# Optimization experiments

Measured on AMD Instinct MI355X. Metric: run time of the kernel, lower is better.

Reference implementation:

```python
import jax, jax.numpy as jnp
import numpy as np

DIM = 1024
HEADS = 16
DIM_HEAD = 64


def setup_inputs() -> dict:
    key = jax.random.key(0)
    ks = jax.random.split(key, 6)
    b, n = 2, 2048
    x = jax.random.normal(ks[0], (b, n, DIM), dtype=jnp.float32)
    gamma = jnp.ones((DIM,), dtype=jnp.float32)
    w_qkv = jax.random.normal(ks[1], (DIM, 3 * HEADS * DIM_HEAD), dtype=jnp.float32) * (DIM ** -0.5)
    w_gates = jax.random.normal(ks[2], (DIM, HEADS), dtype=jnp.float32) * (DIM ** -0.5)
    b_gates = jnp.zeros((HEADS,), dtype=jnp.float32)
    w_out = jax.random.normal(ks[3], (HEADS * DIM_HEAD, DIM), dtype=jnp.float32) * ((HEADS * DIM_HEAD) ** -0.5)
    freqs = jax.random.uniform(ks[4], (DIM_HEAD // 2,), dtype=jnp.float32)
    return {"x": x, "gamma": gamma, "w_qkv": w_qkv, "w_gates": w_gates,
            "b_gates": b_gates, "w_out": w_out, "freqs": freqs}


def _rotate_half(t):
    # interleaved pairs: (x1, x2) -> (-x2, x1)
    tp = t.reshape(t.shape[:-1] + (t.shape[-1] // 2, 2))
    x1, x2 = tp[..., 0], tp[..., 1]
    return jnp.stack((-x2, x1), axis=-1).reshape(t.shape)


def reference(x, gamma, w_qkv, w_gates, b_gates, w_out, freqs):
    b, n, d = x.shape
    # RMSNorm variant: divide by L2 norm, scale by gamma * sqrt(dim)
    xn = x / jnp.linalg.norm(x, axis=-1, keepdims=True)
    xn = xn * gamma * (d ** 0.5)
    # QKV projection: (b, n, 3*H*D) -> q,k,v each (b, h, n, dh)
    qkv = xn @ w_qkv
    qkv = qkv.reshape(b, n, 3, HEADS, DIM_HEAD).transpose(2, 0, 3, 1, 4)
    q, k, v = qkv[0], qkv[1], qkv[2]
    # Inline RoPE (interleaved): freqs (n, dh)
    pos = jnp.arange(n, dtype=freqs.dtype)
    f = jnp.repeat(pos[:, None] * freqs[None, :], 2, axis=-1)  # (n, dh)
    cos_f, sin_f = jnp.cos(f), jnp.sin(f)
    q = q * cos_f + _rotate_half(q) * sin_f
    k = k * cos_f + _rotate_half(k) * sin_f
    # SDPA
    scale = DIM_HEAD ** -0.5
    scores = jnp.einsum('bhqd,bhkd->bhqk', q, k) * scale
    attn = jax.nn.softmax(scores, axis=-1)
    out = jnp.einsum('bhqk,bhkd->bhqd', attn, v)  # (b, h, n, dh)
    # per-head sigmoid gate from normalized input
    gates = xn @ w_gates + b_gates  # (b, n, h)
    out = out * jax.nn.sigmoid(gates.transpose(0, 2, 1))[..., None]
    # merge heads and output projection
    out = out.transpose(0, 2, 1, 3).reshape(b, n, HEADS * DIM_HEAD)
    return out @ w_out
```

## Files before the change

### kernel.cpp

```cpp
#include <hip/hip_runtime.h>

typedef __bf16 bf16_t;
typedef __bf16 bf16x8 __attribute__((ext_vector_type(8)));
typedef __bf16 bf16x4 __attribute__((ext_vector_type(4)));
typedef float f32x4 __attribute__((ext_vector_type(4)));

#define B_  2
#define N_  2048
#define D_  1024
#define H_  16
#define DH_ 64

#define QSCALE 0.18033688011112042f
#define NEGC  -11.541560327111707f

#if __has_builtin(__builtin_amdgcn_exp2f)
#define EXP2F(x) __builtin_amdgcn_exp2f(x)
#else
#define EXP2F(x) exp2f(x)
#endif

#define GLL16(g, l) __builtin_amdgcn_global_load_lds( \
    (const __attribute__((address_space(1))) void*)(g), \
    (__attribute__((address_space(3))) void*)(l), 16, 0, 0)

__device__ __forceinline__ int xcd_swizzle_id() {
  int id = blockIdx.y * gridDim.x + blockIdx.x;
  int cpx = (gridDim.x * gridDim.y) >> 3;
  return (id & 7) * cpx + (id >> 3);
}

__global__ __launch_bounds__(256) void k_prep(
    const float* __restrict__ x, const float* __restrict__ gamma,
    const float* __restrict__ wg, const float* __restrict__ bg,
    bf16_t* __restrict__ xn, float* __restrict__ gsig,
    const float* __restrict__ w_qkv, bf16_t* __restrict__ wqkvT,
    const float* __restrict__ w_out, bf16_t* __restrict__ woutT,
    const float* __restrict__ freqs, float* __restrict__ tc, float* __restrict__ ts) {
  __shared__ __align__(16) char smem_raw[17424];
  int id = blockIdx.x, tid = threadIdx.x;
  if (id < 4096) {
    float* red4 = (float*)smem_raw;
    float (*red)[17] = (float(*)[17])(smem_raw + 16);
    int row = id;
    const float4* xr = (const float4*)(x + (size_t)row * D_);
    float4 v = xr[tid];
    float ss = v.x*v.x + v.y*v.y + v.z*v.z + v.w*v.w;
    #pragma unroll
    for (int off = 32; off > 0; off >>= 1) ss += __shfl_down(ss, off);
    if ((tid & 63) == 0) red4[tid >> 6] = ss;
    __syncthreads();
    float scale = 32.0f * rsqrtf(red4[0] + red4[1] + red4[2] + red4[3]);
    float4 g = ((const float4*)gamma)[tid];
    bf16x4 o;
    o[0] = (bf16_t)(v.x * scale * g.x);
    o[1] = (bf16_t)(v.y * scale * g.y);
    o[2] = (bf16_t)(v.z * scale * g.z);
    o[3] = (bf16_t)(v.w * scale * g.w);
    *(bf16x4*)(xn + (size_t)row * D_ + tid * 4) = o;
    float xv[4] = {(float)o[0], (float)o[1], (float)o[2], (float)o[3]};
    float part[16];
    #pragma unroll
    for (int h = 0; h < 16; ++h) part[h] = 0.f;
    #pragma unroll
    for (int j = 0; j < 4; ++j) {
      const float4* wr = (const float4*)&wg[(size_t)(tid * 4 + j) * 16];
      #pragma unroll
      for (int q = 0; q < 4; ++q) {
        float4 w4 = wr[q];
        part[q * 4 + 0] += xv[j] * w4.x;
        part[q * 4 + 1] += xv[j] * w4.y;
        part[q * 4 + 2] += xv[j] * w4.z;
        part[q * 4 + 3] += xv[j] * w4.w;
      }
    }
    #pragma unroll
    for (int h = 0; h < 16; ++h) red[tid][h] = part[h];
    __syncthreads();
    int h = tid & 15, grp = tid >> 4;
    float s = 0.f;
    #pragma unroll
    for (int k = 0; k < 16; ++k) s += red[grp * 16 + k][h];
    __syncthreads();
    red[grp][h] = s;
    __syncthreads();
    if (tid < 16) {
      float acc = bg[tid];
      #pragma unroll
      for (int k = 0; k < 16; ++k) acc += red[k][tid];
      gsig[(size_t)row * 16 + tid] = 1.0f / (1.0f + __expf(-acc));
    }
  } else if (id < 8192) {
    const float* W; bf16_t* Wt; int R, C, bx, by;
    if (id < 7168) { int local = id - 4096; W = w_qkv; Wt = wqkvT; R = 1024; C = 3072;
                     bx = local % 96; by = local / 96; }
    else           { int local = id - 7168; W = w_out; Wt = woutT; R = 1024; C = 1024;
                     bx = local & 31; by = local >> 5; }
    float (*tile)[33] = (float(*)[33])smem_raw;
    int c0 = bx * 32, r0 = by * 32;
    int tx = tid & 31, ty = tid >> 5;
    #pragma unroll
    for (int i = 0; i < 4; ++i) {
      int r = ty + i * 8;
      tile[r][tx] = W[(size_t)(r0 + r) * C + c0 + tx];
    }
    __syncthreads();
    #pragma unroll
    for (int i = 0; i < 4; ++i) {
      int rr = ty + i * 8;
      Wt[(size_t)(c0 + rr) * R + r0 + tx] = (bf16_t)tile[tx][rr];
    }
  } else {
    int idx = (id - 8192) * 256 + tid;
    int n = idx >> 5, j = idx & 31;
    float f = (float)n * freqs[j];
    tc[idx] = cosf(f);
    ts[idx] = sinf(f);
  }
}

__global__ __launch_bounds__(256) void k_gemm_qkv(const bf16_t* __restrict__ A,
    const bf16_t* __restrict__ Bt, const float* __restrict__ tc,
    const float* __restrict__ ts, bf16_t* __restrict__ Qb,
    bf16_t* __restrict__ Kb, bf16_t* __restrict__ Vb) {
  constexpr int BK = 32, K = 1024;
  constexpr int TP = 136;
  __shared__ __align__(16) char smem[128 * TP * 2];
  bf16_t* As0 = (bf16_t*)smem;
  bf16_t* Bs0 = (bf16_t*)(smem + 16384);
  bf16_t* Tt  = (bf16_t*)smem;
  int tid = threadIdx.x, wave = tid >> 6, lane = tid & 63;
  int l16 = lane & 15, quad = lane >> 4;
  int id = blockIdx.y * 32 + blockIdx.x;
  int xcd = id & 7, local = id >> 3;
  int bxi = (xcd & 3) * 8 + (local & 7);
  int byi = (xcd >> 2) * 12 + (local >> 3);
  int bm = bxi * 128, bn = byi * 128;
  int wm = (wave >> 1) * 64, wn = (wave & 1) * 64;
  int srow = wave * 32 + (lane >> 2);
  int scol = (lane & 3) * 8;
  const bf16_t* gA0 = &A [(size_t)(bm + srow)      * K + scol];
  const bf16_t* gA1 = &A [(size_t)(bm + srow + 16) * K + scol];
  const bf16_t* gB0 = &Bt[(size_t)(bn + srow)      * K + scol];
  const bf16_t* gB1 = &Bt[(size_t)(bn + srow + 16) * K + scol];
  bf16_t* lA0 = &As0[(wave * 32)      * BK];
  bf16_t* lA1 = &As0[(wave * 32 + 16) * BK];
  bf16_t* lB0 = &Bs0[(wave * 32)      * BK];
  bf16_t* lB1 = &Bs0[(wave * 32 + 16) * BK];
  f32x4 acc[4][4] = {};
  GLL16(gA0, lA0); GLL16(gA1, lA1); GLL16(gB0, lB0); GLL16(gB1, lB1);
  __syncthreads();
  for (int k0 = 0; k0 < K; k0 += BK) {
    int cur = (k0 >> 5) & 1;
    int co  = cur * 4096;
    int nxt = 4096 - co;
    if (k0 + BK < K) {
      GLL16(gA0 + k0 + BK, lA0 + nxt);
      GLL16(gA1 + k0 + BK, lA1 + nxt);
      GLL16(gB0 + k0 + BK, lB0 + nxt);
      GLL16(gB1 + k0 + BK, lB1 + nxt);
    }
    const bf16_t* Asc = As0 + co;
    const bf16_t* Bsc = Bs0 + co;
    bf16x8 af[4], bfr[4];
    #pragma unroll
    for (int t = 0; t < 4; ++t) {
      af[t]  = *(const bf16x8*)&Asc[(wm + t * 16 + l16) * BK + quad * 8];
      bfr[t] = *(const bf16x8*)&Bsc[(wn + t * 16 + l16) * BK + quad * 8];
    }
    #pragma unroll
    for (int mt = 0; mt < 4; ++mt)
      #pragma unroll
      for (int nt = 0; nt < 4; ++nt)
        acc[mt][nt] = __builtin_amdgcn_mfma_f32_16x16x32_bf16(af[mt], bfr[nt], acc[mt][nt], 0, 0, 0);
    __syncthreads();
  }
  if (byi < 16) {
    float qs = (byi < 8) ? QSCALE : 1.0f;
    bf16_t* dst = (byi < 8) ? Qb : Kb;
    #pragma unroll
    for (int mt = 0; mt < 4; ++mt)
      #pragma unroll
      for (int r = 0; r < 4; ++r) {
        int row_l = wm + mt * 16 + quad * 4 + r;
        int n = (bm + row_l) & 2047;
        const float* cr = tc + n * 32;
        const float* sr = ts + n * 32;
        #pragma unroll
        for (int nt = 0; nt < 4; ++nt) {
          int col_l = wn + nt * 16 + l16;
          int d = (bn + col_l) & 63, j = d >> 1;
          float val = acc[mt][nt][r];
          float p = __shfl_xor(val, 1);
          float c = cr[j], s = sr[j];
          float o = (d & 1) ? (val * c + p * s) : (val * c - p * s);
          Tt[row_l * TP + col_l] = (bf16_t)(o * qs);
        }
      }
    __syncthreads();
    #pragma unroll
    for (int it = 0; it < 8; ++it) {
      int idx = tid + 256 * it;
      int row_l = idx >> 4, ck = (idx & 15) * 8;
      bf16x8 v = *(const bf16x8*)&Tt[row_l * TP + ck];
      int grow = bm + row_l, b = grow >> 11, n = grow & 2047;
      int col = bn + ck, h = (col >> 6) & 15, d = col & 63;
      *(bf16x8*)&dst[((size_t)(b * H_ + h) * N_ + n) * DH_ + d] = v;
    }
  } else {
    #pragma unroll
    for (int mt = 0; mt < 4; ++mt)
      #pragma unroll
      for (int nt = 0; nt < 4; ++nt) {
        int col_l = wn + nt * 16 + l16;
        int row0 = wm + mt * 16 + quad * 4;
        #pragma unroll
        for (int r = 0; r < 4; ++r)
          Tt[col_l * TP + row0 + r] = (bf16_t)acc[mt][nt][r];
      }
    __syncthreads();
    int b = bm >> 11, nb = bm & 2047;
    #pragma unroll
    for (int it = 0; it < 8; ++it) {
      int idx = tid + 256 * it;
      int col_l = idx >> 4, ck = (idx & 15) * 8;
      bf16x8 v = *(const bf16x8*)&Tt[col_l * TP + ck];
      int vcol = bn + col_l - 2048, h = vcol >> 6, d = vcol & 63;
      *(bf16x8*)&Vb[((size_t)(b * H_ + h) * DH_ + d) * N_ + nb + ck] = v;
    }
  }
}

__global__ __launch_bounds__(256) void k_gemm_bt_n64(const bf16_t* __restrict__ A,
    const bf16_t* __restrict__ Bt, float* __restrict__ C, int M, int N, int K) {
  constexpr int BK = 32;
  __shared__ __align__(16) bf16_t As[128 * BK];
  __shared__ __align__(16) bf16_t Bs[64 * BK];
  int tid = threadIdx.x, wave = tid >> 6, lane = tid & 63;
  int l16 = lane & 15, quad = lane >> 4;
  int swz = xcd_swizzle_id();
  int bxi = swz % gridDim.x, byi = swz / gridDim.x;
  int bm = bxi * 128, bn = byi * 64;
  int wm = (wave >> 1) * 64, wn = (wave & 1) * 32;
  int srow = wave * 32 + (lane >> 2);
  int scol = (lane & 3) * 8;
  const bf16_t* gA0 = &A [(size_t)(bm + srow)      * K + scol];
  const bf16_t* gA1 = &A [(size_t)(bm + srow + 16) * K + scol];
  int srB = wave * 16 + (lane >> 2);
  const bf16_t* gB0 = &Bt[(size_t)(bn + srB) * K + scol];
  bf16_t* lA0 = &As[(wave * 32)      * BK];
  bf16_t* lA1 = &As[(wave * 32 + 16) * BK];
  bf16_t* lB0 = &Bs[(wave * 16)      * BK];
  f32x4 acc[4][2] = {};
  for (int k0 = 0; k0 < K; k0 += BK) {
    GLL16(gA0 + k0, lA0);
    GLL16(gA1 + k0, lA1);
    GLL16(gB0 + k0, lB0);
    __syncthreads();
    bf16x8 af[4], bfr[2];
    #pragma unroll
    for (int t = 0; t < 4; ++t)
      af[t]  = *(const bf16x8*)&As[(wm + t * 16 + l16) * BK + quad * 8];
    #pragma unroll
    for (int t = 0; t < 2; ++t)
      bfr[t] = *(const bf16x8*)&Bs[(wn + t * 16 + l16) * BK + quad * 8];
    #pragma unroll
    for (int mt = 0; mt < 4; ++mt)
      #pragma unroll
      for (int nt = 0; nt < 2; ++nt)
        acc[mt][nt] = __builtin_amdgcn_mfma_f32_16x16x32_bf16(af[mt], bfr[nt], acc[mt][nt], 0, 0, 0);
    __syncthreads();
  }
  #pragma unroll
  for (int mt = 0; mt < 4; ++mt)
    #pragma unroll
    for (int nt = 0; nt < 2; ++nt)
      #pragma unroll
      for (int r = 0; r < 4; ++r) {
        int row = bm + wm + mt * 16 + quad * 4 + r;
        int col = bn + wn + nt * 16 + l16;
        C[(size_t)row * N + col] = acc[mt][nt][r];
      }
}

__global__ __launch_bounds__(256) void k_flash(const bf16_t* __restrict__ Qb,
    const bf16_t* __restrict__ Kb, const bf16_t* __restrict__ Vb,
    const float* __restrict__ gsig, bf16_t* __restrict__ Ao) {
  __shared__ __align__(16) bf16_t Ks[2][64 * 72];
  __shared__ __align__(16) bf16_t Vt[2][64 * 72];
  __shared__ __align__(16) bf16_t Ps[4][32 * 72];
  int swz = xcd_swizzle_id();
  int qblk = swz & 15, bh = swz >> 4;
  int b = bh >> 4, h = bh & 15;
  int tid = threadIdx.x, wave = tid >> 6, lane = tid & 63;
  int l16 = lane & 15, quad = lane >> 4;
  int qw = qblk * 128 + wave * 32;
  const bf16_t* Qh = Qb + (size_t)bh * N_ * DH_;
  const bf16_t* Kh = Kb + (size_t)bh * N_ * DH_;
  const bf16_t* Vh = Vb + (size_t)bh * DH_ * N_;
  bf16_t* Pw = Ps[wave];
  bf16x8 qf[2][2];
  #pragma unroll
  for (int qt = 0; qt < 2; ++qt)
    #pragma unroll
    for (int hf = 0; hf < 2; ++hf)
      qf[qt][hf] = *(const bf16x8*)&Qh[(size_t)(qw + qt * 16 + l16) * DH_ + hf * 32 + quad * 8];
  bf16x8 onesf;
  #pragma unroll
  for (int i = 0; i < 8; ++i) onesf[i] = (bf16_t)1.0f;
  f32x4 accO[2][4] = {};
  f32x4 accL[2] = {};
  int sk = tid >> 3;
  int sc = (tid & 7) * 8;
  bf16x8 rk0 = *(const bf16x8*)&Kh[(size_t)sk * DH_ + sc];
  bf16x8 rk1 = *(const bf16x8*)&Kh[(size_t)(sk + 32) * DH_ + sc];
  bf16x8 rv0 = *(const bf16x8*)&Vh[(size_t)sk * N_ + sc];
  bf16x8 rv1 = *(const bf16x8*)&Vh[(size_t)(sk + 32) * N_ + sc];
  *(bf16x8*)&Ks[0][sk * 72 + sc]        = rk0;
  *(bf16x8*)&Ks[0][(sk + 32) * 72 + sc] = rk1;
  *(bf16x8*)&Vt[0][sk * 72 + sc]        = rv0;
  *(bf16x8*)&Vt[0][(sk + 32) * 72 + sc] = rv1;
  __syncthreads();
  const f32x4 zinit = {NEGC, NEGC, NEGC, NEGC};
  for (int k0 = 0; k0 < N_; k0 += 64) {
    int cur = (k0 >> 6) & 1;
    const bf16_t* Kc = Ks[cur];
    const bf16_t* Vc = Vt[cur];
    int kn = k0 + 64;
    if (kn < N_) {
      rk0 = *(const bf16x8*)&Kh[(size_t)(kn + sk) * DH_ + sc];
      rk1 = *(const bf16x8*)&Kh[(size_t)(kn + sk + 32) * DH_ + sc];
      rv0 = *(const bf16x8*)&Vh[(size_t)sk * N_ + kn + sc];
      rv1 = *(const bf16x8*)&Vh[(size_t)(sk + 32) * N_ + kn + sc];
    }
    f32x4 st[4][2];
    __builtin_amdgcn_s_setprio(1);
    #pragma unroll
    for (int kt = 0; kt < 4; ++kt) {
      bf16x8 kf0 = *(const bf16x8*)&Kc[(kt * 16 + l16) * 72 + quad * 8];
      bf16x8 kf1 = *(const bf16x8*)&Kc[(kt * 16 + l16) * 72 + 32 + quad * 8];
      #pragma unroll
      for (int qt = 0; qt < 2; ++qt) {
        f32x4 z = zinit;
        z = __builtin_amdgcn_mfma_f32_16x16x32_bf16(kf0, qf[qt][0], z, 0, 0, 0);
        z = __builtin_amdgcn_mfma_f32_16x16x32_bf16(kf1, qf[qt][1], z, 0, 0, 0);
        st[kt][qt] = z;
      }
    }
    __builtin_amdgcn_s_setprio(0);
    #pragma unroll
    for (int qt = 0; qt < 2; ++qt)
      #pragma unroll
      for (int kt = 0; kt < 4; ++kt) {
        bf16x4 pk;
        #pragma unroll
        for (int r = 0; r < 4; ++r)
          pk[r] = (bf16_t)EXP2F(st[kt][qt][r]);
        *(bf16x4*)&Pw[(qt * 16 + l16) * 72 + kt * 16 + quad * 4] = pk;
      }
    bf16x8 pf[2][2];
    #pragma unroll
    for (int qt = 0; qt < 2; ++qt)
      #pragma unroll
      for (int hf = 0; hf < 2; ++hf)
        pf[qt][hf] = *(const bf16x8*)&Pw[(qt * 16 + l16) * 72 + hf * 32 + quad * 8];
    __builtin_amdgcn_s_setprio(1);
    #pragma unroll
    for (int qt = 0; qt < 2; ++qt) {
      accL[qt] = __builtin_amdgcn_mfma_f32_16x16x32_bf16(pf[qt][0], onesf, accL[qt], 0, 0, 0);
      accL[qt] = __builtin_amdgcn_mfma_f32_16x16x32_bf16(pf[qt][1], onesf, accL[qt], 0, 0, 0);
    }
    #pragma unroll
    for (int dt = 0; dt < 4; ++dt)
      #pragma unroll
      for (int hf = 0; hf < 2; ++hf) {
        bf16x8 vf = *(const bf16x8*)&Vc[(dt * 16 + l16) * 72 + hf * 32 + quad * 8];
        #pragma unroll
        for (int qt = 0; qt < 2; ++qt)
          accO[qt][dt] = __builtin_amdgcn_mfma_f32_16x16x32_bf16(pf[qt][hf], vf, accO[qt][dt], 0, 0, 0);
      }
    __builtin_amdgcn_s_setprio(0);
    if (kn < N_) {
      int nb = cur ^ 1;
      *(bf16x8*)&Ks[nb][sk * 72 + sc]        = rk0;
      *(bf16x8*)&Ks[nb][(sk + 32) * 72 + sc] = rk1;
      *(bf16x8*)&Vt[nb][sk * 72 + sc]        = rv0;
      *(bf16x8*)&Vt[nb][(sk + 32) * 72 + sc] = rv1;
    }
    __syncthreads();
  }
  #pragma unroll
  for (int qt = 0; qt < 2; ++qt)
    #pragma unroll
    for (int r = 0; r < 4; ++r) {
      int q = qw + qt * 16 + quad * 4 + r;
      float g = gsig[((size_t)b * N_ + q) * H_ + h];
      float ginv = g / accL[qt][r];
      #pragma unroll
      for (int dt = 0; dt < 4; ++dt)
        Ao[((size_t)b * N_ + q) * (H_ * DH_) + h * DH_ + dt * 16 + l16] =
            (bf16_t)(accO[qt][dt][r] * ginv);
    }
}

extern "C" void kernel_launch(void* const* d_in, const int* in_sizes, int n_in,
                              void* d_out, int out_size, void* d_ws, size_t ws_size,
                              hipStream_t stream) {
  (void)in_sizes; (void)n_in; (void)out_size; (void)ws_size;
  const float* x      = (const float*)d_in[0];
  const float* gamma  = (const float*)d_in[1];
  const float* w_qkv  = (const float*)d_in[2];
  const float* w_gate = (const float*)d_in[3];
  const float* b_gate = (const float*)d_in[4];
  const float* w_out  = (const float*)d_in[5];
  const float* freqs  = (const float*)d_in[6];
  float* out = (float*)d_out;
  char* ws = (char*)d_ws;
  bf16_t* xn    = (bf16_t*)(ws);
  bf16_t* wqkvT = (bf16_t*)(ws + ((size_t)8  << 20));
  bf16_t* woutT = (bf16_t*)(ws + ((size_t)14 << 20));
  bf16_t* Qb    = (bf16_t*)(ws + ((size_t)16 << 20));
  bf16_t* Kb    = (bf16_t*)(ws + ((size_t)24 << 20));
  bf16_t* Vb    = (bf16_t*)(ws + ((size_t)32 << 20));
  float*  gsig  = (float*) (ws + ((size_t)40 << 20));
  bf16_t* attn  = (bf16_t*)(ws + ((size_t)41 << 20));
  float*  trigc = (float*) (ws + ((size_t)49 << 20));
  float*  trigs = (float*) (ws + ((size_t)50 << 20));

  k_prep<<<8448, 256, 0, stream>>>(x, gamma, w_gate, b_gate, xn, gsig,
                                   w_qkv, wqkvT, w_out, woutT, freqs, trigc, trigs);
  k_gemm_qkv<<<dim3(32, 24), 256, 0, stream>>>(xn, wqkvT, trigc, trigs, Qb, Kb, Vb);
  k_flash<<<dim3(16, 32), 256, 0, stream>>>(Qb, Kb, Vb, gsig, attn);
  k_gemm_bt_n64<<<dim3(32, 16), 256, 0, stream>>>(attn, woutT, out, 4096, 1024, 1024);
}
```

Before: 224.9 us.

## Double-buffer LDS in output-projection GEMM and remap blocks per XCD

Doubles the shared-memory tiles in the N=64 GEMM and prefetches the next K-slice with global_load_lds while MFMAs run on the current one, removing the load-then-sync stall in each iteration. It also replaces the generic XCD swizzle with a hardcoded mapping that groups 8x8 tiles per XCD for L2 reuse. The mapping assumes a 32-wide grid with a fixed shape, and the loop's synchronisation must still cover the asynchronous LDS writes.

```diff
diff --git a/kernel.cpp b/kernel.cpp
--- a/kernel.cpp
+++ b/kernel.cpp
@@ -234,12 +234,14 @@
 __global__ __launch_bounds__(256) void k_gemm_bt_n64(const bf16_t* __restrict__ A,
     const bf16_t* __restrict__ Bt, float* __restrict__ C, int M, int N, int K) {
   constexpr int BK = 32;
-  __shared__ __align__(16) bf16_t As[128 * BK];
-  __shared__ __align__(16) bf16_t Bs[64 * BK];
+  __shared__ __align__(16) bf16_t As0[128 * BK * 2];
+  __shared__ __align__(16) bf16_t Bs0[64 * BK * 2];
   int tid = threadIdx.x, wave = tid >> 6, lane = tid & 63;
   int l16 = lane & 15, quad = lane >> 4;
-  int swz = xcd_swizzle_id();
-  int bxi = swz % gridDim.x, byi = swz / gridDim.x;
+  int id = blockIdx.y * 32 + blockIdx.x;
+  int xcd = id & 7, local = id >> 3;
+  int bxi = (xcd & 3) * 8 + (local & 7);
+  int byi = (xcd >> 2) * 8 + (local >> 3);
   int bm = bxi * 128, bn = byi * 64;
   int wm = (wave >> 1) * 64, wn = (wave & 1) * 32;
   int srow = wave * 32 + (lane >> 2);
@@ -248,22 +250,30 @@
   const bf16_t* gA1 = &A [(size_t)(bm + srow + 16) * K + scol];
   int srB = wave * 16 + (lane >> 2);
   const bf16_t* gB0 = &Bt[(size_t)(bn + srB) * K + scol];
-  bf16_t* lA0 = &As[(wave * 32)      * BK];
-  bf16_t* lA1 = &As[(wave * 32 + 16) * BK];
-  bf16_t* lB0 = &Bs[(wave * 16)      * BK];
+  bf16_t* lA0 = &As0[(wave * 32)      * BK];
+  bf16_t* lA1 = &As0[(wave * 32 + 16) * BK];
+  bf16_t* lB0 = &Bs0[(wave * 16)      * BK];
   f32x4 acc[4][2] = {};
+  GLL16(gA0, lA0); GLL16(gA1, lA1); GLL16(gB0, lB0);
+  __syncthreads();
   for (int k0 = 0; k0 < K; k0 += BK) {
-    GLL16(gA0 + k0, lA0);
-    GLL16(gA1 + k0, lA1);
-    GLL16(gB0 + k0, lB0);
-    __syncthreads();
+    int cur = (k0 >> 5) & 1;
+    int coA = cur * 4096, nxA = 4096 - coA;
+    int coB = cur * 2048, nxB = 2048 - coB;
+    if (k0 + BK < K) {
+      GLL16(gA0 + k0 + BK, lA0 + nxA);
+      GLL16(gA1 + k0 + BK, lA1 + nxA);
+      GLL16(gB0 + k0 + BK, lB0 + nxB);
+    }
+    const bf16_t* Asc = As0 + coA;
+    const bf16_t* Bsc = Bs0 + coB;
     bf16x8 af[4], bfr[2];
     #pragma unroll
     for (int t = 0; t < 4; ++t)
-      af[t]  = *(const bf16x8*)&As[(wm + t * 16 + l16) * BK + quad * 8];
+      af[t]  = *(const bf16x8*)&Asc[(wm + t * 16 + l16) * BK + quad * 8];
     #pragma unroll
     for (int t = 0; t < 2; ++t)
-      bfr[t] = *(const bf16x8*)&Bs[(wn + t * 16 + l16) * BK + quad * 8];
+      bfr[t] = *(const bf16x8*)&Bsc[(wn + t * 16 + l16) * BK + quad * 8];
     #pragma unroll
     for (int mt = 0; mt < 4; ++mt)
       #pragma unroll
```

After: 219.8 us (median of 2 runs). 1.02x faster.
